# Kernel tuning notes

Hardware: AMD Instinct MI355X
Metric: run time of the kernel (lower is better)

## Reference

```python
import jax, jax.numpy as jnp
import numpy as np

D_MODEL = 1024
N_HEADS = 16
HEAD_DIM = D_MODEL // N_HEADS
NEG = -10000.0  # module uses -10000, not -inf


def setup_inputs() -> dict:
    key = jax.random.key(0)
    ks = jax.random.split(key, 8)
    B, T = 4, 2048
    q = jax.random.normal(ks[0], (B, T, D_MODEL), dtype=jnp.float32)
    k = jax.random.normal(ks[1], (B, T, D_MODEL), dtype=jnp.float32)
    v = jax.random.normal(ks[2], (B, T, D_MODEL), dtype=jnp.float32)
    attn_mask = jnp.ones((B, T), dtype=jnp.float32)
    # xavier_uniform for square [d, d] weights: limit = sqrt(6/(d+d))
    lim = float(np.sqrt(6.0 / (D_MODEL + D_MODEL)))
    Wq = jax.random.uniform(ks[3], (D_MODEL, D_MODEL), jnp.float32, -lim, lim)
    Wk = jax.random.uniform(ks[4], (D_MODEL, D_MODEL), jnp.float32, -lim, lim)
    Wv = jax.random.uniform(ks[5], (D_MODEL, D_MODEL), jnp.float32, -lim, lim)
    Wo = jax.random.uniform(ks[6], (D_MODEL, D_MODEL), jnp.float32, -lim, lim)
    return {"q": q, "k": k, "v": v, "attn_mask": attn_mask,
            "Wq": Wq, "Wk": Wk, "Wv": Wv, "Wo": Wo, "mask_future": 1}


def _split_heads(x):
    B, T, _ = x.shape
    return x.reshape(B, T, N_HEADS, HEAD_DIM).transpose(0, 2, 1, 3)  # [B,H,T,D]


def reference(q, k, v, attn_mask, Wq, Wk, Wv, Wo, mask_future):
    # torch Linear: y = x @ W.T  (weights stored [out, in])
    qh = _split_heads(jnp.einsum('btd,ed->bte', q, Wq))
    kh = _split_heads(jnp.einsum('btd,ed->bte', k, Wk))
    vh = _split_heads(jnp.einsum('btd,ed->bte', v, Wv))
    L, S = qh.shape[-2], kh.shape[-2]
    # dual scale: each of q and k scaled by 1/d**0.25
    scale = 1.0 / jnp.sqrt(jnp.sqrt(jnp.float32(HEAD_DIM)))
    scores = jnp.einsum('bhld,bhsd->bhls', qh * scale, kh * scale)
    if mask_future:
        causal_bias = jnp.triu(jnp.full((L, S), NEG, dtype=scores.dtype), k=1)
        scores = scores + causal_bias
    # padding mask: attn_mask [B, S] -> broadcast [B,1,1,S]; 0 entries -> -10000
    pad = attn_mask[:, None, None, :]
    scores = jnp.where(pad == 0, jnp.asarray(NEG, scores.dtype), scores)
    probs = jax.nn.softmax(scores, axis=-1)  # dropout p=0.0 -> identity
    ctx = jnp.einsum('bhls,bhsd->bhld', probs, vh)
    B = ctx.shape[0]
    ctx = ctx.transpose(0, 2, 1, 3).reshape(B, L, D_MODEL)
    return jnp.einsum('btd,ed->bte', ctx, Wo)
```

## Files before the change

kernel.cpp:

```cpp
#include <hip/hip_runtime.h>

typedef unsigned short u16;
typedef __attribute__((ext_vector_type(8))) _Float16 f16x8;
typedef __attribute__((ext_vector_type(2))) __fp16 fp16v2;
typedef __attribute__((ext_vector_type(4))) float f32x4;
typedef __attribute__((ext_vector_type(16))) float f32x16;

#define T_SEQ 2048
#define NH 16
#define DH 64
#define DM 1024
#define NEG2 (-14426.95f)
#define QS2 (0.42466089f)

__device__ __forceinline__ unsigned pk2(float a, float b) {
  union { fp16v2 v; unsigned u; } c;
  c.v = __builtin_amdgcn_cvt_pkrtz(a, b);
  return c.u;
}
__device__ __forceinline__ u16 f2h(float a) {
  union { _Float16 h; u16 u; } c; c.h = (_Float16)a; return c.u;
}

__device__ __forceinline__ void async_load16(const void* g, void* l) {
  __builtin_amdgcn_global_load_lds(
      (const __attribute__((address_space(1))) unsigned int*)(g),
      (__attribute__((address_space(3))) unsigned int*)(l), 16, 0, 0);
}

__global__ __launch_bounds__(256) void convert_all(
    const float* __restrict__ q, const float* __restrict__ k, const float* __restrict__ v,
    const float* __restrict__ Wq, const float* __restrict__ Wk, const float* __restrict__ Wv,
    const float* __restrict__ Wo, u16* __restrict__ xb, u16* __restrict__ wb) {
  int blk = blockIdx.x;
  const float* src; u16* dst;
  if (blk < 12288) {
    int s = blk >> 12;
    src = (s == 0) ? q : (s == 1) ? k : v;
    dst = xb + (size_t)s * 8388608u;
    blk &= 4095;
  } else {
    int s = (blk - 12288) >> 9;
    src = (s == 0) ? Wq : (s == 1) ? Wk : (s == 2) ? Wv : Wo;
    dst = wb + (size_t)s * 1048576u;
    blk = (blk - 12288) & 511;
  }
  size_t base = (size_t)blk * 2048 + (size_t)threadIdx.x * 8;
  float4 a = *(const float4*)(src + base);
  float4 b2 = *(const float4*)(src + base + 4);
  uint4 st;
  st.x = pk2(a.x, a.y); st.y = pk2(a.z, a.w);
  st.z = pk2(b2.x, b2.y); st.w = pk2(b2.z, b2.w);
  *(uint4*)(dst + base) = st;
}

__global__ __launch_bounds__(256) void gemm_qkv(const u16* __restrict__ A,
                                                const u16* __restrict__ Wqb,
                                                const u16* __restrict__ Wkb,
                                                const u16* __restrict__ Wvb,
                                                u16* __restrict__ Qh, u16* __restrict__ Kh,
                                                u16* __restrict__ VTh) {
  __shared__ char lds[33792];
  const int tid = threadIdx.x;
  const int wid = tid >> 6, lane = tid & 63;
  const int l32 = lane & 31, lh = lane >> 5;
  const int m0 = blockIdx.x * 128;
  const int n0 = blockIdx.y * 128;
  const int which = n0 >> 10;
  const int n0l = n0 & 1023;
  const u16* As = A + (size_t)which * 8388608u;
  const u16* Bw = (which == 0) ? Wqb : (which == 1) ? Wkb : Wvb;
  const int wm = wid >> 1, wn = wid & 1;
  f32x16 acc[2][2] = {};

  const u16* gA = As + (size_t)(m0 + wid * 32 + l32) * 1024 + lh * 8;
  const u16* gB = Bw + (size_t)(n0l + wid * 32 + l32) * 1024 + lh * 8;
  async_load16(gA, lds + (wid * 2 + 0) * 1024);
  async_load16(gA + 16, lds + (wid * 2 + 1) * 1024);
  async_load16(gB, lds + 8192 + (wid * 2 + 0) * 1024);
  async_load16(gB + 16, lds + 8192 + (wid * 2 + 1) * 1024);

  for (int it = 0; it < 32; ++it) {
    __syncthreads();
    char* cur = lds + (it & 1) * 16384;
    if (it < 31) {
      char* nxt = lds + ((it + 1) & 1) * 16384;
      int kt = (it + 1) * 32;
      async_load16(gA + kt, nxt + (wid * 2 + 0) * 1024);
      async_load16(gA + kt + 16, nxt + (wid * 2 + 1) * 1024);
      async_load16(gB + kt, nxt + 8192 + (wid * 2 + 0) * 1024);
      async_load16(gB + kt + 16, nxt + 8192 + (wid * 2 + 1) * 1024);
    }
    char* const rb = (which < 2) ? (cur + 8192) : cur;
    char* const cb = (which < 2) ? cur : (cur + 8192);
    for (int ks = 0; ks < 2; ++ks) {
      f16x8 rf[2], cf[2];
      for (int i = 0; i < 2; ++i) {
        rf[i] = *(const f16x8*)(rb + ((wm * 2 + i) * 2 + ks) * 1024 + lane * 16);
        cf[i] = *(const f16x8*)(cb + ((wn * 2 + i) * 2 + ks) * 1024 + lane * 16);
      }
      for (int i = 0; i < 2; ++i)
        for (int j = 0; j < 2; ++j)
          acc[i][j] = __builtin_amdgcn_mfma_f32_32x32x16_f16(rf[i], cf[j], acc[i][j], 0, 0, 0);
    }
  }

  const float s = (which < 2) ? QS2 : 1.0f;
  __syncthreads();
  for (int i = 0; i < 2; ++i)
    for (int j = 0; j < 2; ++j) {
      int colb = wn * 64 + j * 32 + l32;
      int rowb = wm * 64 + i * 32 + 4 * lh;
      for (int g = 0; g < 4; ++g) {
        uint2 pv;
        pv.x = pk2(acc[i][j][4 * g + 0] * s, acc[i][j][4 * g + 1] * s);
        pv.y = pk2(acc[i][j][4 * g + 2] * s, acc[i][j][4 * g + 3] * s);
        *(uint2*)(lds + colb * 264 + (rowb + 8 * g) * 2) = pv;
      }
    }
  __syncthreads();

  const int b = m0 >> 11, t0 = m0 & 2047, h0 = n0l >> 6;
  if (which < 2) {
    u16* O = which ? Kh : Qh;
    for (int p = 0; p < 8; ++p) {
      int row = p * 16 + (tid >> 4);
      int seg = tid & 15;
      uint4 val = *(const uint4*)(lds + row * 264 + seg * 16);
      int hl = seg >> 3, dh0 = (seg & 7) * 8;
      *(uint4*)(O + (((size_t)(b * NH + h0 + hl) * T_SEQ + t0 + row) << 6) + dh0) = val;
    }
  } else {
    for (int p = 0; p < 8; ++p) {
      int row = p * 16 + (tid >> 4);
      int seg = tid & 15;
      uint4 val = *(const uint4*)(lds + row * 264 + seg * 16);
      int h = h0 + (row >> 6), dh = row & 63;
      *(uint4*)(VTh + (((size_t)(b * NH + h) * DH + dh) << 11) + t0 + seg * 8) = val;
    }
  }
}

__global__ __launch_bounds__(256) void gemm_out(const u16* __restrict__ A,
                                                const u16* __restrict__ Bw,
                                                float* __restrict__ O) {
  __shared__ char lds[32768];
  const int tid = threadIdx.x;
  const int wid = tid >> 6, lane = tid & 63;
  const int l32 = lane & 31, lh = lane >> 5;
  const int m0 = blockIdx.x * 128, n0 = blockIdx.y * 128;
  const int wm = wid >> 1, wn = wid & 1;
  f32x16 acc[2][2] = {};

  const u16* gA = A + (size_t)(m0 + wid * 32 + l32) * 1024 + lh * 8;
  const u16* gB = Bw + (size_t)(n0 + wid * 32 + l32) * 1024 + lh * 8;
  async_load16(gA, lds + (wid * 2 + 0) * 1024);
  async_load16(gA + 16, lds + (wid * 2 + 1) * 1024);
  async_load16(gB, lds + 8192 + (wid * 2 + 0) * 1024);
  async_load16(gB + 16, lds + 8192 + (wid * 2 + 1) * 1024);

  for (int it = 0; it < 32; ++it) {
    __syncthreads();
    char* cur = lds + (it & 1) * 16384;
    if (it < 31) {
      char* nxt = lds + ((it + 1) & 1) * 16384;
      int kt = (it + 1) * 32;
      async_load16(gA + kt, nxt + (wid * 2 + 0) * 1024);
      async_load16(gA + kt + 16, nxt + (wid * 2 + 1) * 1024);
      async_load16(gB + kt, nxt + 8192 + (wid * 2 + 0) * 1024);
      async_load16(gB + kt + 16, nxt + 8192 + (wid * 2 + 1) * 1024);
    }
    for (int ks = 0; ks < 2; ++ks) {
      f16x8 af[2], bf[2];
      for (int i = 0; i < 2; ++i) {
        af[i] = *(const f16x8*)(cur + ((wm * 2 + i) * 2 + ks) * 1024 + lane * 16);
        bf[i] = *(const f16x8*)(cur + 8192 + ((wn * 2 + i) * 2 + ks) * 1024 + lane * 16);
      }
      for (int i = 0; i < 2; ++i)
        for (int j = 0; j < 2; ++j)
          acc[i][j] = __builtin_amdgcn_mfma_f32_32x32x16_f16(af[i], bf[j], acc[i][j], 0, 0, 0);
    }
  }
  for (int i = 0; i < 2; ++i)
    for (int j = 0; j < 2; ++j) {
      int col = n0 + wn * 64 + j * 32 + l32;
      int rowb = m0 + wm * 64 + i * 32 + 4 * lh;
      for (int g = 0; g < 4; ++g)
        for (int rr = 0; rr < 4; ++rr)
          O[(size_t)(rowb + 8 * g + rr) * 1024 + col] = acc[i][j][4 * g + rr];
    }
}

__global__ __launch_bounds__(512) void attn_kernel(const u16* __restrict__ Qh,
                                                   const u16* __restrict__ Kh,
                                                   const u16* __restrict__ VTh,
                                                   const float* __restrict__ attn_mask,
                                                   const int* __restrict__ mfp,
                                                   u16* __restrict__ ctx) {
  __shared__ char kls[8192];
  __shared__ char vls[8192];
  __shared__ char pls[8][2048];
  __shared__ float maskb[T_SEQ];
  __shared__ int mzf;

  const int tid = threadIdx.x;
  const int wid = tid >> 6, lane = tid & 63;
  const int lm = lane & 15, lq = lane >> 4;
  const int bid = blockIdx.x;
  const int bh_i = bid & 63, p8 = bid >> 6;
  const int b = bh_i >> 4, h = bh_i & 15;
  const int mf = *mfp;
  const size_t bh = (size_t)(b * NH + h);
  const u16* Qbh = Qh + bh * T_SEQ * DH;
  const u16* Kbh = Kh + bh * T_SEQ * DH;
  const u16* VTbh = VTh + bh * DH * T_SEQ;

  if (tid == 0) mzf = 0;
  __syncthreads();
  {
    int az = 0;
    for (int i = tid; i < T_SEQ; i += 512) {
      float mv = attn_mask[(size_t)b * T_SEQ + i];
      maskb[i] = (mv == 0.0f) ? NEG2 : 0.0f;
      az |= (mv == 0.0f);
    }
    if (az) mzf = 1;
  }
  __syncthreads();
  const int maskzero = mzf;

  for (int half = 0; half < 2; ++half) {
    const int qt = half ? (15 - p8) : p8;
    const int q0 = qt * 128;
    const int qw = q0 + wid * 16;
    f16x8 qf[2];
    qf[0] = *(const f16x8*)(Qbh + (size_t)(qw + lm) * DH + lq * 8);
    qf[1] = *(const f16x8*)(Qbh + (size_t)(qw + lm) * DH + 32 + lq * 8);

    f32x4 acc[4] = {};
    float mprev = -1e30f, lsum = 0.f;

    const int nch = mf ? (qt + 1) * 2 : 32;
    for (int c = 0; c < nch; ++c) {
      const int s0 = c * 64;
      __syncthreads();
      async_load16(Kbh + (size_t)(s0 + (wid >> 1) * 16 + lm) * DH + (wid & 1) * 32 + lq * 8,
                   kls + wid * 1024);
      async_load16(VTbh + (size_t)((wid >> 1) * 16 + lm) * T_SEQ + s0 + (wid & 1) * 32 + lq * 8,
                   vls + wid * 1024);
      __syncthreads();

      f32x4 sc[4];
      for (int st = 0; st < 4; ++st) {
        f32x4 z = {0.f, 0.f, 0.f, 0.f};
        sc[st] = z;
        for (int kk = 0; kk < 2; ++kk) {
          f16x8 kf = *(const f16x8*)(kls + ((st * 2 + kk) * 64 + lane) * 16);
          sc[st] = __builtin_amdgcn_mfma_f32_16x16x32_f16(kf, qf[kk], sc[st], 0, 0, 0);
        }
      }
      if (maskzero) {
        for (int st = 0; st < 4; ++st) {
          f32x4 mb = *(const f32x4*)(maskb + s0 + st * 16 + lq * 4);
          for (int r = 0; r < 4; ++r) sc[st][r] += mb[r];
        }
      }
      if (mf && (s0 + 64 > qw)) {
        int qg = qw + lm;
        for (int st = 0; st < 4; ++st)
          for (int r = 0; r < 4; ++r)
            if (s0 + st * 16 + lq * 4 + r > qg) sc[st][r] = NEG2;
      }
      float mx = fmaxf(fmaxf(sc[0][0], sc[0][1]), fmaxf(sc[0][2], sc[0][3]));
      for (int st = 1; st < 4; ++st) {
        float t2 = fmaxf(fmaxf(sc[st][0], sc[st][1]), fmaxf(sc[st][2], sc[st][3]));
        mx = fmaxf(mx, t2);
      }
      mx = fmaxf(mx, __shfl_xor(mx, 16));
      mx = fmaxf(mx, __shfl_xor(mx, 32));
      float mn = mprev;
      if (__ballot(mx > mprev) != 0ull) {
        mn = fmaxf(mprev, mx);
        float alpha = exp2f(mprev - mn);
        for (int r = 0; r < 4; ++r) {
          float ar = __shfl(alpha, lq * 4 + r);
          for (int nt = 0; nt < 4; ++nt) acc[nt][r] *= ar;
        }
        lsum *= alpha;
        mprev = mn;
      }
      float ps = 0.f;
      for (int st = 0; st < 4; ++st)
        for (int r = 0; r < 4; ++r) {
          float p = exp2f(sc[st][r] - mn);
          sc[st][r] = p;
          ps += p;
        }
      ps += __shfl_xor(ps, 16);
      ps += __shfl_xor(ps, 32);
      lsum += ps;
      {
        char* pw = pls[wid];
        for (int st = 0; st < 4; ++st) {
          int kk = st >> 1;
          int lqp = (st & 1) * 2 + (lq >> 1);
          uint2 pv;
          pv.x = pk2(sc[st][0], sc[st][1]);
          pv.y = pk2(sc[st][2], sc[st][3]);
          *(uint2*)(pw + kk * 1024 + (lqp * 16 + lm) * 16 + (lq & 1) * 8) = pv;
        }
      }
      asm volatile("s_waitcnt lgkmcnt(0)" ::: "memory");
      for (int kk = 0; kk < 2; ++kk) {
        f16x8 pf = *(const f16x8*)(pls[wid] + kk * 1024 + lane * 16);
        for (int nt = 0; nt < 4; ++nt) {
          f16x8 vf = *(const f16x8*)(vls + ((nt * 2 + kk) * 64 + lane) * 16);
          acc[nt] = __builtin_amdgcn_mfma_f32_16x16x32_f16(pf, vf, acc[nt], 0, 0, 0);
        }
      }
    }
    float inv = 1.0f / lsum;
    for (int r = 0; r < 4; ++r) {
      float ir = __shfl(inv, lq * 4 + r);
      int t = qw + lq * 4 + r;
      for (int nt = 0; nt < 4; ++nt)
        ctx[((size_t)(b * T_SEQ + t) * DM) + h * DH + nt * 16 + lm] = f2h(acc[nt][r] * ir);
    }
  }
}

extern "C" void kernel_launch(void* const* d_in, const int* in_sizes, int n_in,
                              void* d_out, int out_size, void* d_ws, size_t ws_size,
                              hipStream_t stream) {
  const float* q = (const float*)d_in[0];
  const float* k = (const float*)d_in[1];
  const float* v = (const float*)d_in[2];
  const float* attn_mask = (const float*)d_in[3];
  const float* Wq = (const float*)d_in[4];
  const float* Wk = (const float*)d_in[5];
  const float* Wv = (const float*)d_in[6];
  const float* Wo = (const float*)d_in[7];
  const int* mf = (const int*)d_in[8];

  u16* ws = (u16*)d_ws;
  u16* qb  = ws;
  u16* wqb = ws + 3u * 8388608u;
  u16* wkb = wqb + 1048576u;
  u16* wvb = wkb + 1048576u;
  u16* wob = wvb + 1048576u;
  u16* Qh  = wob + 1048576u;
  u16* Kh  = Qh + 8388608u;
  u16* VTh = Kh + 8388608u;
  u16* ctxb = ws;

  convert_all<<<14336, 256, 0, stream>>>(q, k, v, Wq, Wk, Wv, Wo, qb, wqb);

  dim3 gq(64, 24);
  gemm_qkv<<<gq, 256, 0, stream>>>(qb, wqb, wkb, wvb, Qh, Kh, VTh);

  attn_kernel<<<512, 512, 0, stream>>>(Qh, Kh, VTh, attn_mask, mf, ctxb);

  dim3 gg(64, 8);
  gemm_out<<<gg, 256, 0, stream>>>(ctxb, wob, (float*)d_out);
}
```

Before: 371.1 us.

## Triple-buffer GEMM K-loop with explicit vmcnt waits and early-release prefetch

Both the QKV projection GEMM and the output GEMM move from a double-buffered LDS pipeline to a three-stage ring buffer, prefetching two K-tiles ahead. Fine-grained s_waitcnt vmcnt counts replace the full __syncthreads wait. All fragments for the current tile are loaded into registers before a second barrier, which frees the buffer so the next async load can overwrite it while the MFMAs run. This aims to hide global-load latency better, at the cost of more LDS per block (48KB), which may lower occupancy, and an extra barrier per iteration.

```diff
diff --git a/kernel.cpp b/kernel.cpp
--- a/kernel.cpp
+++ b/kernel.cpp
@@ -60,7 +60,7 @@
                                                 const u16* __restrict__ Wvb,
                                                 u16* __restrict__ Qh, u16* __restrict__ Kh,
                                                 u16* __restrict__ VTh) {
-  __shared__ char lds[33792];
+  __shared__ char lds[49152];
   const int tid = threadIdx.x;
   const int wid = tid >> 6, lane = tid & 63;
   const int l32 = lane & 31, lh = lane >> 5;
@@ -75,34 +75,46 @@
 
   const u16* gA = As + (size_t)(m0 + wid * 32 + l32) * 1024 + lh * 8;
   const u16* gB = Bw + (size_t)(n0l + wid * 32 + l32) * 1024 + lh * 8;
-  async_load16(gA, lds + (wid * 2 + 0) * 1024);
-  async_load16(gA + 16, lds + (wid * 2 + 1) * 1024);
-  async_load16(gB, lds + 8192 + (wid * 2 + 0) * 1024);
-  async_load16(gB + 16, lds + 8192 + (wid * 2 + 1) * 1024);
-
+  for (int t = 0; t < 3; ++t) {
+    char* bf = lds + t * 16384;
+    async_load16(gA + t * 32, bf + (wid * 2 + 0) * 1024);
+    async_load16(gA + t * 32 + 16, bf + (wid * 2 + 1) * 1024);
+    async_load16(gB + t * 32, bf + 8192 + (wid * 2 + 0) * 1024);
+    async_load16(gB + t * 32 + 16, bf + 8192 + (wid * 2 + 1) * 1024);
+  }
+
+  int buf = 0;
   for (int it = 0; it < 32; ++it) {
-    __syncthreads();
-    char* cur = lds + (it & 1) * 16384;
-    if (it < 31) {
-      char* nxt = lds + ((it + 1) & 1) * 16384;
-      int kt = (it + 1) * 32;
-      async_load16(gA + kt, nxt + (wid * 2 + 0) * 1024);
-      async_load16(gA + kt + 16, nxt + (wid * 2 + 1) * 1024);
-      async_load16(gB + kt, nxt + 8192 + (wid * 2 + 0) * 1024);
-      async_load16(gB + kt + 16, nxt + 8192 + (wid * 2 + 1) * 1024);
-    }
+    if (it < 30)       asm volatile("s_waitcnt vmcnt(8)" ::: "memory");
+    else if (it == 30) asm volatile("s_waitcnt vmcnt(4)" ::: "memory");
+    else               asm volatile("s_waitcnt vmcnt(0)" ::: "memory");
+    __builtin_amdgcn_s_barrier();
+    asm volatile("" ::: "memory");
+    char* cur = lds + buf * 16384;
     char* const rb = (which < 2) ? (cur + 8192) : cur;
     char* const cb = (which < 2) ? cur : (cur + 8192);
-    for (int ks = 0; ks < 2; ++ks) {
-      f16x8 rf[2], cf[2];
+    f16x8 rf[2][2], cf[2][2];
+    for (int ks = 0; ks < 2; ++ks)
       for (int i = 0; i < 2; ++i) {
-        rf[i] = *(const f16x8*)(rb + ((wm * 2 + i) * 2 + ks) * 1024 + lane * 16);
-        cf[i] = *(const f16x8*)(cb + ((wn * 2 + i) * 2 + ks) * 1024 + lane * 16);
-      }
+        rf[ks][i] = *(const f16x8*)(rb + ((wm * 2 + i) * 2 + ks) * 1024 + lane * 16);
+        cf[ks][i] = *(const f16x8*)(cb + ((wn * 2 + i) * 2 + ks) * 1024 + lane * 16);
+      }
+    if (it < 29) {
+      asm volatile("s_waitcnt lgkmcnt(0)" ::: "memory");
+      __builtin_amdgcn_sched_barrier(0);
+      __builtin_amdgcn_s_barrier();
+      asm volatile("" ::: "memory");
+      int kt = (it + 3) * 32;
+      async_load16(gA + kt, cur + (wid * 2 + 0) * 1024);
+      async_load16(gA + kt + 16, cur + (wid * 2 + 1) * 1024);
+      async_load16(gB + kt, cur + 8192 + (wid * 2 + 0) * 1024);
+      async_load16(gB + kt + 16, cur + 8192 + (wid * 2 + 1) * 1024);
+    }
+    for (int ks = 0; ks < 2; ++ks)
       for (int i = 0; i < 2; ++i)
         for (int j = 0; j < 2; ++j)
-          acc[i][j] = __builtin_amdgcn_mfma_f32_32x32x16_f16(rf[i], cf[j], acc[i][j], 0, 0, 0);
-    }
+          acc[i][j] = __builtin_amdgcn_mfma_f32_32x32x16_f16(rf[ks][i], cf[ks][j], acc[i][j], 0, 0, 0);
+    buf = (buf == 2) ? 0 : buf + 1;
   }
 
   const float s = (which < 2) ? QS2 : 1.0f;
@@ -144,7 +156,7 @@
 __global__ __launch_bounds__(256) void gemm_out(const u16* __restrict__ A,
                                                 const u16* __restrict__ Bw,
                                                 float* __restrict__ O) {
-  __shared__ char lds[32768];
+  __shared__ char lds[49152];
   const int tid = threadIdx.x;
   const int wid = tid >> 6, lane = tid & 63;
   const int l32 = lane & 31, lh = lane >> 5;
@@ -154,32 +166,44 @@
 
   const u16* gA = A + (size_t)(m0 + wid * 32 + l32) * 1024 + lh * 8;
   const u16* gB = Bw + (size_t)(n0 + wid * 32 + l32) * 1024 + lh * 8;
-  async_load16(gA, lds + (wid * 2 + 0) * 1024);
-  async_load16(gA + 16, lds + (wid * 2 + 1) * 1024);
-  async_load16(gB, lds + 8192 + (wid * 2 + 0) * 1024);
-  async_load16(gB + 16, lds + 8192 + (wid * 2 + 1) * 1024);
-
+  for (int t = 0; t < 3; ++t) {
+    char* bf = lds + t * 16384;
+    async_load16(gA + t * 32, bf + (wid * 2 + 0) * 1024);
+    async_load16(gA + t * 32 + 16, bf + (wid * 2 + 1) * 1024);
+    async_load16(gB + t * 32, bf + 8192 + (wid * 2 + 0) * 1024);
+    async_load16(gB + t * 32 + 16, bf + 8192 + (wid * 2 + 1) * 1024);
+  }
+
+  int buf = 0;
   for (int it = 0; it < 32; ++it) {
-    __syncthreads();
-    char* cur = lds + (it & 1) * 16384;
-    if (it < 31) {
-      char* nxt = lds + ((it + 1) & 1) * 16384;
-      int kt = (it + 1) * 32;
-      async_load16(gA + kt, nxt + (wid * 2 + 0) * 1024);
-      async_load16(gA + kt + 16, nxt + (wid * 2 + 1) * 1024);
-      async_load16(gB + kt, nxt + 8192 + (wid * 2 + 0) * 1024);
-      async_load16(gB + kt + 16, nxt + 8192 + (wid * 2 + 1) * 1024);
-    }
-    for (int ks = 0; ks < 2; ++ks) {
-      f16x8 af[2], bf[2];
+    if (it < 30)       asm volatile("s_waitcnt vmcnt(8)" ::: "memory");
+    else if (it == 30) asm volatile("s_waitcnt vmcnt(4)" ::: "memory");
+    else               asm volatile("s_waitcnt vmcnt(0)" ::: "memory");
+    __builtin_amdgcn_s_barrier();
+    asm volatile("" ::: "memory");
+    char* cur = lds + buf * 16384;
+    f16x8 af[2][2], bf2[2][2];
+    for (int ks = 0; ks < 2; ++ks)
       for (int i = 0; i < 2; ++i) {
-        af[i] = *(const f16x8*)(cur + ((wm * 2 + i) * 2 + ks) * 1024 + lane * 16);
-        bf[i] = *(const f16x8*)(cur + 8192 + ((wn * 2 + i) * 2 + ks) * 1024 + lane * 16);
-      }
+        af[ks][i] = *(const f16x8*)(cur + ((wm * 2 + i) * 2 + ks) * 1024 + lane * 16);
+        bf2[ks][i] = *(const f16x8*)(cur + 8192 + ((wn * 2 + i) * 2 + ks) * 1024 + lane * 16);
+      }
+    if (it < 29) {
+      asm volatile("s_waitcnt lgkmcnt(0)" ::: "memory");
+      __builtin_amdgcn_sched_barrier(0);
+      __builtin_amdgcn_s_barrier();
+      asm volatile("" ::: "memory");
+      int kt = (it + 3) * 32;
+      async_load16(gA + kt, cur + (wid * 2 + 0) * 1024);
+      async_load16(gA + kt + 16, cur + (wid * 2 + 1) * 1024);
+      async_load16(gB + kt, cur + 8192 + (wid * 2 + 0) * 1024);
+      async_load16(gB + kt + 16, cur + 8192 + (wid * 2 + 1) * 1024);
+    }
+    for (int ks = 0; ks < 2; ++ks)
       for (int i = 0; i < 2; ++i)
         for (int j = 0; j < 2; ++j)
-          acc[i][j] = __builtin_amdgcn_mfma_f32_32x32x16_f16(af[i], bf[j], acc[i][j], 0, 0, 0);
-    }
+          acc[i][j] = __builtin_amdgcn_mfma_f32_32x32x16_f16(af[ks][i], bf2[ks][j], acc[i][j], 0, 0, 0);
+    buf = (buf == 2) ? 0 : buf + 1;
   }
   for (int i = 0; i < 2; ++i)
     for (int j = 0; j < 2; ++j) {
```

Result: no change. 371.1 us (+0.0%).
